# Optimization experiments

Hardware: AMD Instinct MI355X
Metric: run time of the kernel (lower is better)

Reference implementation:

```python
import jax, jax.numpy as jnp
import numpy as np

ED = 200      # entity/relation dim
KW = 9        # kernel width
OC = 32       # out channels
WOUT = ED - KW + 1  # 192 valid-conv output width
B = 1024
NE = 40943
NR = 18


def setup_inputs() -> dict:
    key = jax.random.key(0)
    ks = jax.random.split(key, 9)
    g = lambda k, shape: jax.random.normal(k, shape, jnp.float32) * 0.05
    return dict(
        e1_idx=jax.random.randint(ks[0], (B,), 0, NE, dtype=jnp.int32),
        r_idx=jax.random.randint(ks[1], (B,), 0, NR, dtype=jnp.int32),
        W1=g(ks[2], (ED, KW * OC)),
        b1=g(ks[3], (KW * OC,)),
        W2=g(ks[4], (WOUT * OC, ED)),
        b2=g(ks[5], (ED,)),
        bias_logits=g(ks[6], (NE,)),
        E=g(ks[7], (NE, ED)),
        R=g(ks[8], (NR, ED)),
    )


def reference(e1_idx, r_idx, W1, b1, W2, b2, bias_logits, E, R):
    e1 = E[e1_idx]          # [B, 200]
    r = R[r_idx]            # [B, 200]
    # hypernetwork: relation -> per-sample conv filters [B, KW, OC]
    k = (r @ W1 + b1).reshape(-1, KW, OC)
    # per-sample valid 1D conv of e1 with its own filters (depthwise-as-groups trick collapsed)
    idx = jnp.arange(WOUT)[:, None] + jnp.arange(KW)[None, :]  # [WOUT, KW]
    patches = e1[:, idx]                                        # [B, WOUT, KW]
    # flatten order matches TF: (out_channel major, width minor)
    feat = jnp.einsum('bwj,bjo->bow', patches, k).reshape(e1.shape[0], OC * WOUT)
    h = jax.nn.relu(feat @ W2 + b2)                             # [B, 200]
    logits = h @ E.T + bias_logits                              # [B, NE]
    return logits
```

## Files before the change

kernel.cpp:

```cpp
#include <hip/hip_runtime.h>

#define NE 40943
#define NR 18
#define ED 200
#define KWC 9
#define OC 32
#define WOUT 192
#define KOC 288
#define KH 224

typedef unsigned short u16;
typedef unsigned int u32;
typedef __bf16 bf16x8 __attribute__((ext_vector_type(8)));
typedef float f32x4 __attribute__((ext_vector_type(4)));
typedef u16 u16x8 __attribute__((ext_vector_type(8)));
typedef u16 u16x4 __attribute__((ext_vector_type(4)));

__device__ __forceinline__ u16 f2bf(float f) {
  u32 u = __builtin_bit_cast(u32, f);
  u32 r = (u + 0x7fffu + ((u >> 16) & 1u)) >> 16;
  return (u16)r;
}

__device__ __forceinline__ void gl_lds16(const u16* g, u16* l) {
  __builtin_amdgcn_global_load_lds(
      (const __attribute__((address_space(1))) u32*)g,
      (__attribute__((address_space(3))) u32*)l, 16, 0, 0);
}

__global__ void prep_k_kernel(const float* __restrict__ R,
                              const float* __restrict__ W1,
                              const float* __restrict__ b1,
                              float* __restrict__ KrT) {
  int rel = blockIdx.x;
  int j = threadIdx.x;
  float acc = b1[j];
  const float* rrow = R + rel * ED;
  for (int d = 0; d < ED; ++d) acc += rrow[d] * W1[d * KOC + j];
  KrT[j * NR + rel] = acc;
}

__global__ __launch_bounds__(256) void build_c_kernel(const float* __restrict__ KrT,
                                                      const float* __restrict__ W2,
                                                      float* __restrict__ C) {
  int p = blockIdx.x;
  int d = threadIdx.x;
  int jlo = p > (WOUT - 1) ? p - (WOUT - 1) : 0;
  int jhi = p < (KWC - 1) ? p : (KWC - 1);
  if (d < ED) {
    float acc[NR];
#pragma unroll
    for (int r = 0; r < NR; ++r) acc[r] = 0.f;
    for (int j = jlo; j <= jhi; ++j) {
      int w = p - j;
      const float* w2base = W2 + (size_t)w * ED + d;
      const float* kb = KrT + (j * OC) * NR;
#pragma unroll
      for (int o = 0; o < OC; ++o) {
        float w2v = w2base[(size_t)o * WOUT * ED];
#pragma unroll
        for (int r = 0; r < NR; ++r) acc[r] += kb[o * NR + r] * w2v;
      }
    }
#pragma unroll
    for (int r = 0; r < NR; ++r) C[((size_t)r * ED + p) * ED + d] = acc[r];
  }
}

__global__ __launch_bounds__(256) void h_kernel(const int* __restrict__ e1_idx,
                                                const int* __restrict__ r_idx,
                                                const float* __restrict__ E,
                                                const float* __restrict__ C,
                                                const float* __restrict__ b2,
                                                u16* __restrict__ Hb) {
  __shared__ float e1s[ED];
  int b = blockIdx.x;
  int t = threadIdx.x;
  if (t < ED) e1s[t] = E[(size_t)e1_idx[b] * ED + t];
  __syncthreads();
  int r = r_idx[b];
  const float* Cr = C + (size_t)r * ED * ED;
  if (t < KH) {
    float acc = 0.f;
    if (t < ED) {
#pragma unroll 8
      for (int p = 0; p < ED; ++p) acc += e1s[p] * Cr[(size_t)p * ED + t];
      acc += b2[t];
      acc = acc > 0.f ? acc : 0.f;
    }
    Hb[(size_t)b * KH + t] = (t < ED) ? f2bf(acc) : (u16)0;
  }
}

__global__ void conv_e_kernel(const float* __restrict__ E, u16* __restrict__ Eb) {
  int idx = blockIdx.x * 256 + threadIdx.x;
  const int total = NE * (KH / 4);
  if (idx >= total) return;
  int row = idx / (KH / 4);
  int c4 = (idx % (KH / 4)) * 4;
  u16x4 st = {0, 0, 0, 0};
  if (c4 < ED) {
    f32x4 v = *(const f32x4*)(E + (size_t)row * ED + c4);
    st[0] = f2bf(v[0]); st[1] = f2bf(v[1]); st[2] = f2bf(v[2]); st[3] = f2bf(v[3]);
  }
  *(u16x4*)(Eb + (size_t)row * KH + c4) = st;
}

__global__ __launch_bounds__(256) void gemm2_kernel(
    const u16* __restrict__ Hb,
    const u16* __restrict__ Eb,
    const float* __restrict__ bias,
    float* __restrict__ out) {
  __shared__ __align__(16) u16 lA[2][128 * 32];
  __shared__ __align__(16) u16 lB[2][128 * 32];
  const int t = threadIdx.x;
  const int wave = t >> 6, lane = t & 63;

  int id = blockIdx.x;
  int xcd = id & 7;
  int q = id >> 3;
  int bx = xcd * 40 + q % 40;
  int by = q / 40;
  const int m0 = by * 128;
  const int n0 = bx * 128;
  const int wm = (wave >> 1) * 64, wn = (wave & 1) * 64;
  const int lr = lane & 15, lq = lane >> 4;
  const int csw = (lq ^ ((lr >> 1) & 3)) * 8;

  int aoff[2], boff[2], loff[2];
#pragma unroll
  for (int s = 0; s < 2; ++s) {
    int chunk = wave * 128 + s * 64 + lane;
    int r = chunk >> 2, cc = chunk & 3;
    int ccs = cc ^ ((r >> 1) & 3);
    loff[s] = chunk * 8;
    aoff[s] = (m0 + r) * KH + ccs * 8;
    int gr = n0 + r;
    if (gr > NE - 1) gr = NE - 1;
    boff[s] = gr * KH + ccs * 8;
  }

  f32x4 zero = {0.f, 0.f, 0.f, 0.f};
  f32x4 acc[4][4];
#pragma unroll
  for (int i = 0; i < 4; ++i)
#pragma unroll
    for (int j = 0; j < 4; ++j) acc[i][j] = zero;

#pragma unroll
  for (int s = 0; s < 2; ++s) {
    gl_lds16(Hb + aoff[s], &lA[0][loff[s]]);
    gl_lds16(Eb + boff[s], &lB[0][loff[s]]);
  }
  __syncthreads();

  int cur = 0;
  for (int kt = 0; kt < KH / 32; ++kt) {
    if (kt < KH / 32 - 1) {
      int k0 = (kt + 1) * 32;
#pragma unroll
      for (int s = 0; s < 2; ++s) {
        gl_lds16(Hb + aoff[s] + k0, &lA[cur ^ 1][loff[s]]);
        gl_lds16(Eb + boff[s] + k0, &lB[cur ^ 1][loff[s]]);
      }
    }
    bf16x8 af[4], bfv[4];
#pragma unroll
    for (int mi = 0; mi < 4; ++mi) {
      int rr = wm + mi * 16 + lr;
      af[mi] = *(const bf16x8*)(&lA[cur][rr * 32 + csw]);
    }
#pragma unroll
    for (int ni = 0; ni < 4; ++ni) {
      int rr = wn + ni * 16 + lr;
      bfv[ni] = *(const bf16x8*)(&lB[cur][rr * 32 + csw]);
    }
#pragma unroll
    for (int mi = 0; mi < 4; ++mi)
#pragma unroll
      for (int ni = 0; ni < 4; ++ni)
        acc[mi][ni] = __builtin_amdgcn_mfma_f32_16x16x32_bf16(af[mi], bfv[ni], acc[mi][ni], 0, 0, 0);
    __syncthreads();
    cur ^= 1;
  }

#pragma unroll
  for (int mi = 0; mi < 4; ++mi) {
    int row = m0 + wm + mi * 16 + lq * 4;
#pragma unroll
    for (int ni = 0; ni < 4; ++ni) {
      int col = n0 + wn + ni * 16 + lr;
      if (col < NE) {
        float bv = bias[col];
#pragma unroll
        for (int i = 0; i < 4; ++i)
          out[(size_t)(row + i) * NE + col] = acc[mi][ni][i] + bv;
      }
    }
  }
}

extern "C" void kernel_launch(void* const* d_in, const int* in_sizes, int n_in,
                              void* d_out, int out_size, void* d_ws, size_t ws_size,
                              hipStream_t stream) {
  const int* e1_idx = (const int*)d_in[0];
  const int* r_idx = (const int*)d_in[1];
  const float* W1 = (const float*)d_in[2];
  const float* b1 = (const float*)d_in[3];
  const float* W2 = (const float*)d_in[4];
  const float* b2 = (const float*)d_in[5];
  const float* bias_logits = (const float*)d_in[6];
  const float* E = (const float*)d_in[7];
  const float* R = (const float*)d_in[8];
  float* out = (float*)d_out;

  char* ws = (char*)d_ws;
  float* KrT = (float*)ws;
  float* C = (float*)(ws + 32768);
  u16* Hb = (u16*)(ws + 32768 + 2880000);
  u16* Eb = (u16*)(ws + 32768 + 2880000 + 458752);

  prep_k_kernel<<<dim3(NR), dim3(KOC), 0, stream>>>(R, W1, b1, KrT);
  build_c_kernel<<<dim3(ED), dim3(256), 0, stream>>>(KrT, W2, C);
  h_kernel<<<dim3(1024), dim3(256), 0, stream>>>(e1_idx, r_idx, E, C, b2, Hb);
  conv_e_kernel<<<dim3((NE * (KH / 4) + 255) / 256), dim3(256), 0, stream>>>(E, Eb);
  gemm2_kernel<<<dim3(320 * 8), dim3(256), 0, stream>>>(Hb, Eb, bias_logits, out);
}
```

Baseline: 309.5 us.

## Fuse relation-filter prep into C build, split OC reduction, widen conversions

The separate prep kernel is removed. Each build_c block now recomputes the 18x288 relation filter table into shared memory, then splits the 32 output channels across two 256-thread halves and combines the two partial sums through LDS. The h kernel uses four independent accumulators to shorten its dependency chain, and the E-to-bf16 conversion handles eight elements per thread with 16-byte stores. This trims one launch and adds parallelism to the C build, at the cost of every one of the 200 blocks redundantly computing the filter table (18x200x288 MACs each).

```diff
diff --git a/kernel.cpp b/kernel.cpp
--- a/kernel.cpp
+++ b/kernel.cpp
@@ -28,42 +28,61 @@
       (__attribute__((address_space(3))) u32*)l, 16, 0, 0);
 }
 
-__global__ void prep_k_kernel(const float* __restrict__ R,
-                              const float* __restrict__ W1,
-                              const float* __restrict__ b1,
-                              float* __restrict__ KrT) {
-  int rel = blockIdx.x;
-  int j = threadIdx.x;
-  float acc = b1[j];
-  const float* rrow = R + rel * ED;
-  for (int d = 0; d < ED; ++d) acc += rrow[d] * W1[d * KOC + j];
-  KrT[j * NR + rel] = acc;
-}
-
-__global__ __launch_bounds__(256) void build_c_kernel(const float* __restrict__ KrT,
+__global__ __launch_bounds__(512) void build_c_kernel(const float* __restrict__ R,
+                                                      const float* __restrict__ W1,
+                                                      const float* __restrict__ b1,
                                                       const float* __restrict__ W2,
                                                       float* __restrict__ C) {
-  int p = blockIdx.x;
-  int d = threadIdx.x;
-  int jlo = p > (WOUT - 1) ? p - (WOUT - 1) : 0;
-  int jhi = p < (KWC - 1) ? p : (KWC - 1);
+  __shared__ float krt[KOC * NR];
+  __shared__ float partial[NR * ED];
+  const int t = threadIdx.x;
+  const int p = blockIdx.x;
+
+  if (t < KOC) {
+    const int col = t;
+    float acc[NR];
+#pragma unroll
+    for (int r = 0; r < NR; ++r) acc[r] = 0.f;
+    for (int d = 0; d < ED; ++d) {
+      float w1v = W1[d * KOC + col];
+#pragma unroll
+      for (int r = 0; r < NR; ++r) acc[r] += R[r * ED + d] * w1v;
+    }
+    float b1v = b1[col];
+#pragma unroll
+    for (int r = 0; r < NR; ++r) krt[col * NR + r] = acc[r] + b1v;
+  }
+  __syncthreads();
+
+  const int y = t >> 8;
+  const int d = t & 255;
+  const int jlo = p > (WOUT - 1) ? p - (WOUT - 1) : 0;
+  const int jhi = p < (KWC - 1) ? p : (KWC - 1);
+  float accC[NR];
+#pragma unroll
+  for (int r = 0; r < NR; ++r) accC[r] = 0.f;
   if (d < ED) {
-    float acc[NR];
-#pragma unroll
-    for (int r = 0; r < NR; ++r) acc[r] = 0.f;
     for (int j = jlo; j <= jhi; ++j) {
       int w = p - j;
-      const float* w2base = W2 + (size_t)w * ED + d;
-      const float* kb = KrT + (j * OC) * NR;
-#pragma unroll
-      for (int o = 0; o < OC; ++o) {
-        float w2v = w2base[(size_t)o * WOUT * ED];
-#pragma unroll
-        for (int r = 0; r < NR; ++r) acc[r] += kb[o * NR + r] * w2v;
-      }
-    }
-#pragma unroll
-    for (int r = 0; r < NR; ++r) C[((size_t)r * ED + p) * ED + d] = acc[r];
+      const float* w2base = W2 + (size_t)w * ED + d + (size_t)(y * 16) * WOUT * ED;
+      const float* kb = krt + (j * OC + y * 16) * NR;
+#pragma unroll
+      for (int oo = 0; oo < 16; ++oo) {
+        float w2v = w2base[(size_t)oo * WOUT * ED];
+#pragma unroll
+        for (int r = 0; r < NR; ++r) accC[r] += kb[oo * NR + r] * w2v;
+      }
+    }
+  }
+  if (y == 1 && d < ED) {
+#pragma unroll
+    for (int r = 0; r < NR; ++r) partial[r * ED + d] = accC[r];
+  }
+  __syncthreads();
+  if (y == 0 && d < ED) {
+#pragma unroll
+    for (int r = 0; r < NR; ++r)
+      C[((size_t)r * ED + p) * ED + d] = accC[r] + partial[r * ED + d];
   }
 }
 
@@ -83,9 +102,15 @@
   if (t < KH) {
     float acc = 0.f;
     if (t < ED) {
-#pragma unroll 8
-      for (int p = 0; p < ED; ++p) acc += e1s[p] * Cr[(size_t)p * ED + t];
-      acc += b2[t];
+      float a0 = 0.f, a1 = 0.f, a2 = 0.f, a3 = 0.f;
+#pragma unroll 4
+      for (int p = 0; p < ED; p += 4) {
+        a0 += e1s[p + 0] * Cr[(size_t)(p + 0) * ED + t];
+        a1 += e1s[p + 1] * Cr[(size_t)(p + 1) * ED + t];
+        a2 += e1s[p + 2] * Cr[(size_t)(p + 2) * ED + t];
+        a3 += e1s[p + 3] * Cr[(size_t)(p + 3) * ED + t];
+      }
+      acc = ((a0 + a1) + (a2 + a3)) + b2[t];
       acc = acc > 0.f ? acc : 0.f;
     }
     Hb[(size_t)b * KH + t] = (t < ED) ? f2bf(acc) : (u16)0;
@@ -94,16 +119,18 @@
 
 __global__ void conv_e_kernel(const float* __restrict__ E, u16* __restrict__ Eb) {
   int idx = blockIdx.x * 256 + threadIdx.x;
-  const int total = NE * (KH / 4);
+  const int total = NE * (KH / 8);
   if (idx >= total) return;
-  int row = idx / (KH / 4);
-  int c4 = (idx % (KH / 4)) * 4;
-  u16x4 st = {0, 0, 0, 0};
-  if (c4 < ED) {
-    f32x4 v = *(const f32x4*)(E + (size_t)row * ED + c4);
-    st[0] = f2bf(v[0]); st[1] = f2bf(v[1]); st[2] = f2bf(v[2]); st[3] = f2bf(v[3]);
-  }
-  *(u16x4*)(Eb + (size_t)row * KH + c4) = st;
+  int row = idx / (KH / 8);
+  int c8 = (idx % (KH / 8)) * 8;
+  u16x8 st = {0, 0, 0, 0, 0, 0, 0, 0};
+  if (c8 < ED) {
+    f32x4 v0 = *(const f32x4*)(E + (size_t)row * ED + c8);
+    f32x4 v1 = *(const f32x4*)(E + (size_t)row * ED + c8 + 4);
+    st[0] = f2bf(v0[0]); st[1] = f2bf(v0[1]); st[2] = f2bf(v0[2]); st[3] = f2bf(v0[3]);
+    st[4] = f2bf(v1[0]); st[5] = f2bf(v1[1]); st[6] = f2bf(v1[2]); st[7] = f2bf(v1[3]);
+  }
+  *(u16x8*)(Eb + (size_t)row * KH + c8) = st;
 }
 
 __global__ __launch_bounds__(256) void gemm2_kernel(
@@ -215,14 +242,12 @@
   float* out = (float*)d_out;
 
   char* ws = (char*)d_ws;
-  float* KrT = (float*)ws;
   float* C = (float*)(ws + 32768);
   u16* Hb = (u16*)(ws + 32768 + 2880000);
   u16* Eb = (u16*)(ws + 32768 + 2880000 + 458752);
 
-  prep_k_kernel<<<dim3(NR), dim3(KOC), 0, stream>>>(R, W1, b1, KrT);
-  build_c_kernel<<<dim3(ED), dim3(256), 0, stream>>>(KrT, W2, C);
+  build_c_kernel<<<dim3(ED), dim3(512), 0, stream>>>(R, W1, b1, W2, C);
   h_kernel<<<dim3(1024), dim3(256), 0, stream>>>(e1_idx, r_idx, E, C, b2, Hb);
-  conv_e_kernel<<<dim3((NE * (KH / 4) + 255) / 256), dim3(256), 0, stream>>>(E, Eb);
+  conv_e_kernel<<<dim3((NE * (KH / 8) + 255) / 256), dim3(256), 0, stream>>>(E, Eb);
   gemm2_kernel<<<dim3(320 * 8), dim3(256), 0, stream>>>(Hb, Eb, bias_logits, out);
 }
```

After: 329.7 us. 1.07x slower.
